# Kernel tuning notes

Measured on AMD Instinct MI355X. Metric: run time of the kernel, lower is better.

## Reference

```python
import jax, jax.numpy as jnp
import numpy as np

K = 3  # Chebyshev order (number of coefficients)


def setup_inputs() -> dict:
    key = jax.random.key(0)
    k1, k2, k3, k4 = jax.random.split(key, 4)
    B, nNode, c_in, T = 16, 512, 32, 64
    c_out = 64
    x = jax.random.normal(k1, (B, nNode, c_in, T), dtype=jnp.float32)
    # scaled Laplacian-like batched adjacency; scale keeps the Chebyshev
    # recursion numerically tame (spectral norm ~ O(1))
    adj = jax.random.normal(k2, (B, nNode, nNode), dtype=jnp.float32) * (1.0 / np.sqrt(nNode))
    # 1x1 conv params: weight [c_out, K*c_in], bias [c_out]
    W = jax.random.normal(k3, (c_out, K * c_in), dtype=jnp.float32) * 0.1
    b = jax.random.normal(k4, (c_out,), dtype=jnp.float32) * 0.1
    return {"x": x, "adj": adj, "W": W, "b": b}


def reference(x, adj, W, b):
    # x: [B, nNode, c_in, T] -> permute(0,2,1,3) -> [B, c_in, nNode, T]
    x = jnp.transpose(x, (0, 2, 1, 3))
    B, c_in, nNode, T = x.shape
    # Chebyshev recursion: L0 = I, L1 = adj, L_k = 2*adj@L_{k-1} - L_{k-2}
    L0 = jnp.broadcast_to(jnp.eye(nNode, dtype=x.dtype), (B, nNode, nNode))
    L1 = adj
    Ls = [L0, L1]
    for _ in range(2, K):
        L2 = 2.0 * jnp.matmul(adj, L1) - L0
        L0, L1 = L1, L2
        Ls.append(L2)
    Lap = jnp.stack(Ls, axis=1)              # [B, K, nNode, nNode]
    Lap = jnp.swapaxes(Lap, -1, -2)          # transpose(-1, -2)
    # einsum 'bcnl,bknq->bckql' then view [B, c_in*K, nNode, T]
    y = jnp.einsum('bcnl,bknq->bckql', x, Lap)  # [B, c_in, K, nNode, T]
    y = y.reshape(B, c_in * K, nNode, T)
    # 1x1 Conv2d: channel mixing + bias
    out = jnp.einsum('oc,bcnl->bonl', W, y) + b[None, :, None, None]
    return out
```

## Files before the change

### kernel.cpp

```cpp
#include <hip/hip_runtime.h>

typedef unsigned short u16;
typedef __bf16 v8bf __attribute__((ext_vector_type(8)));
typedef float f32x4 __attribute__((ext_vector_type(4)));
typedef u16 us8 __attribute__((ext_vector_type(8)));

static __device__ __forceinline__ u16 f2bf(float f) {
  union { __bf16 h; u16 u; } cv;
  cv.h = (__bf16)f;
  return cv.u;
}

__global__ __launch_bounds__(256)
void cvt_f2bf_k(const float* __restrict__ in, u16* __restrict__ out, int n8) {
  const int i = blockIdx.x * 256 + threadIdx.x;
  if (i >= n8) return;
  const float4 a = ((const float4*)in)[2 * i];
  const float4 b = ((const float4*)in)[2 * i + 1];
  us8 r;
  r[0] = f2bf(a.x); r[1] = f2bf(a.y); r[2] = f2bf(a.z); r[3] = f2bf(a.w);
  r[4] = f2bf(b.x); r[5] = f2bf(b.y); r[6] = f2bf(b.z); r[7] = f2bf(b.w);
  ((us8*)out)[i] = r;
}

__global__ __launch_bounds__(256)
void foldw_k(const float* __restrict__ W, u16* __restrict__ Mb) {
  const int i = blockIdx.x * 256 + threadIdx.x;
  if (i >= 64 * 96) return;
  const int cc = i % 96;
  const int r = cc % 3;
  const float w = W[i];
  const float m = (r == 0) ? (w - W[i + 2]) : ((r == 1) ? w : 2.0f * w);
  Mb[i] = f2bf(m);
}

#define BM 128
#define BN 128
#define BK 32

__global__ __launch_bounds__(256)
void gemm_bf16(const u16* __restrict__ A, const u16* __restrict__ Bm,
               u16* __restrict__ C) {
  const int b = blockIdx.z;
  const int row0 = blockIdx.y * BM;
  const int col0 = blockIdx.x * BN;
  const u16* Ab = A + (size_t)b * 512 * 512;
  const u16* Bb = Bm + (size_t)b * 512 * 2048;
  u16* Cb = C + (size_t)b * 512 * 2048;

  __shared__ u16 As[BM][BK + 8];
  __shared__ u16 Bs[BN][BK + 8];

  const int tid = threadIdx.x;
  const int lane = tid & 63;
  const int w = tid >> 6;
  const int wm = (w >> 1) * 64;
  const int wn = (w & 1) * 64;
  const int l16 = lane & 15;
  const int kg = lane >> 4;

  f32x4 acc[4][4];
#pragma unroll
  for (int m = 0; m < 4; ++m)
#pragma unroll
    for (int n = 0; n < 4; ++n)
      acc[m][n] = (f32x4){0.f, 0.f, 0.f, 0.f};

  for (int k0 = 0; k0 < 512; k0 += BK) {
#pragma unroll
    for (int i = 0; i < 2; ++i) {
      const int idx = tid + 256 * i;
      const int r = idx >> 2;
      const int ka = (idx & 3) * 8;
      *(uint4*)&As[r][ka] = *(const uint4*)(Ab + (size_t)(row0 + r) * 512 + k0 + ka);
    }
#pragma unroll
    for (int i = 0; i < 2; ++i) {
      const int idx = tid + 256 * i;
      const int n = idx & 127;
      const int kb = (idx >> 7) * 8;
      const u16* src = Bb + (size_t)(k0 + kb) * 2048 + col0 + n;
      us8 v;
#pragma unroll
      for (int j = 0; j < 8; ++j) v[j] = src[(size_t)j * 2048];
      *(us8*)&Bs[n][kb] = v;
    }
    __syncthreads();
    v8bf af[4], bfr[4];
#pragma unroll
    for (int m = 0; m < 4; ++m) af[m] = *(const v8bf*)&As[wm + m * 16 + l16][kg * 8];
#pragma unroll
    for (int n = 0; n < 4; ++n) bfr[n] = *(const v8bf*)&Bs[wn + n * 16 + l16][kg * 8];
#pragma unroll
    for (int m = 0; m < 4; ++m)
#pragma unroll
      for (int n = 0; n < 4; ++n)
        acc[m][n] = __builtin_amdgcn_mfma_f32_16x16x32_bf16(af[m], bfr[n], acc[m][n], 0, 0, 0);
    __syncthreads();
  }
#pragma unroll
  for (int m = 0; m < 4; ++m)
#pragma unroll
    for (int n = 0; n < 4; ++n)
#pragma unroll
      for (int v = 0; v < 4; ++v) {
        const int rr = row0 + wm + m * 16 + kg * 4 + v;
        const int cc = col0 + wn + n * 16 + l16;
        Cb[(size_t)rr * 2048 + cc] = f2bf(acc[m][n][v]);
      }
}

__global__ __launch_bounds__(256)
void mix_mfma(const float* __restrict__ x0, const u16* __restrict__ x1,
              const u16* __restrict__ y2, const u16* __restrict__ Mb,
              const float* __restrict__ bias, float* __restrict__ out) {
  const int q = blockIdx.x;
  const int b = blockIdx.y;
  __shared__ u16 Vt[64][104];
  __shared__ u16 Ms[64][104];
  const int tid = threadIdx.x;
  const int lane = tid & 63;
  const int w = tid >> 6;
  const int l16 = lane & 15;
  const int kg = lane >> 4;

#pragma unroll
  for (int i = 0; i < 3; ++i) {
    const int idx = tid + 256 * i;
    const int o = idx / 12;
    const int c8 = (idx % 12) * 8;
    *(uint4*)&Ms[o][c8] = *(const uint4*)(Mb + o * 96 + c8);
  }
  const size_t base = ((size_t)b * 512 + q) * 2048;
#pragma unroll
  for (int i = 0; i < 2; ++i) {
    const int idx = tid + 256 * i;
    const int c = idx >> 4;
    const int l0 = (idx & 15) * 4;
    const float4 v = *(const float4*)(x0 + base + c * 64 + l0);
    Vt[l0 + 0][3 * c] = f2bf(v.x);
    Vt[l0 + 1][3 * c] = f2bf(v.y);
    Vt[l0 + 2][3 * c] = f2bf(v.z);
    Vt[l0 + 3][3 * c] = f2bf(v.w);
  }
  {
    const int c = tid >> 3;
    const int l0 = (tid & 7) * 8;
    const us8 v1 = *(const us8*)(x1 + base + c * 64 + l0);
    const us8 v2 = *(const us8*)(y2 + base + c * 64 + l0);
#pragma unroll
    for (int j = 0; j < 8; ++j) {
      Vt[l0 + j][3 * c + 1] = v1[j];
      Vt[l0 + j][3 * c + 2] = v2[j];
    }
  }
  __syncthreads();

  f32x4 acc[4];
#pragma unroll
  for (int n = 0; n < 4; ++n) acc[n] = (f32x4){0.f, 0.f, 0.f, 0.f};
#pragma unroll
  for (int ks = 0; ks < 3; ++ks) {
    const v8bf a = *(const v8bf*)&Ms[w * 16 + l16][ks * 32 + kg * 8];
#pragma unroll
    for (int n = 0; n < 4; ++n) {
      const v8bf bv = *(const v8bf*)&Vt[n * 16 + l16][ks * 32 + kg * 8];
      acc[n] = __builtin_amdgcn_mfma_f32_16x16x32_bf16(a, bv, acc[n], 0, 0, 0);
    }
  }
#pragma unroll
  for (int n = 0; n < 4; ++n)
#pragma unroll
    for (int v = 0; v < 4; ++v) {
      const int o = w * 16 + kg * 4 + v;
      out[(((size_t)b * 64 + o) * 512 + q) * 64 + n * 16 + l16] = acc[n][v] + bias[o];
    }
}

extern "C" void kernel_launch(void* const* d_in, const int* in_sizes, int n_in,
                              void* d_out, int out_size, void* d_ws, size_t ws_size,
                              hipStream_t stream) {
  const float* x   = (const float*)d_in[0];
  const float* adj = (const float*)d_in[1];
  const float* W   = (const float*)d_in[2];
  const float* bia = (const float*)d_in[3];
  float* out = (float*)d_out;

  u16* adj_bf = (u16*)d_ws;
  u16* x_bf   = adj_bf + (size_t)16 * 512 * 512;
  u16* X1     = x_bf   + (size_t)16 * 512 * 2048;
  u16* Y2     = X1     + (size_t)16 * 512 * 2048;
  u16* Mb     = Y2     + (size_t)16 * 512 * 2048;

  const int n8_adj = 16 * 512 * 512 / 8;
  const int n8_x   = 16 * 512 * 2048 / 8;
  hipLaunchKernelGGL(cvt_f2bf_k, dim3(n8_adj / 256), dim3(256), 0, stream, adj, adj_bf, n8_adj);
  hipLaunchKernelGGL(cvt_f2bf_k, dim3(n8_x / 256), dim3(256), 0, stream, x, x_bf, n8_x);
  hipLaunchKernelGGL(foldw_k, dim3(24), dim3(256), 0, stream, W, Mb);

  dim3 gg(2048 / BN, 512 / BM, 16);
  hipLaunchKernelGGL(gemm_bf16, gg, dim3(256), 0, stream, adj_bf, x_bf, X1);
  hipLaunchKernelGGL(gemm_bf16, gg, dim3(256), 0, stream, adj_bf, X1, Y2);

  hipLaunchKernelGGL(mix_mfma, dim3(512, 16), dim3(256), 0, stream, x, X1, Y2, Mb, bia, out);
}
```

Baseline: 151.2 us.

## Store GEMM B operands transposed and load tiles via global_load_lds

x is converted to bf16 in a transposed [B,2048,512] layout, and the first GEMM also writes a transposed copy of X1. Both GEMMs can then fetch K-contiguous tiles with direct global-to-LDS 16-byte loads (BK=64) instead of strided 2-byte gathers across 2048-wide rows. The adj conversion and weight folding are merged into one launch. The cost is an extra transpose pass through LDS, an extra X1T write, and unpadded LDS tiles that may cause bank conflicts.

Result: slower. 158.5 us (+4.8%).

```diff
diff --git a/kernel.cpp b/kernel.cpp
--- a/kernel.cpp
+++ b/kernel.cpp
@@ -4,6 +4,7 @@
 typedef __bf16 v8bf __attribute__((ext_vector_type(8)));
 typedef float f32x4 __attribute__((ext_vector_type(4)));
 typedef u16 us8 __attribute__((ext_vector_type(8)));
+typedef u16 us4 __attribute__((ext_vector_type(4)));
 
 static __device__ __forceinline__ u16 f2bf(float f) {
   union { __bf16 h; u16 u; } cv;
@@ -11,45 +12,77 @@
   return cv.u;
 }
 
-__global__ __launch_bounds__(256)
-void cvt_f2bf_k(const float* __restrict__ in, u16* __restrict__ out, int n8) {
-  const int i = blockIdx.x * 256 + threadIdx.x;
-  if (i >= n8) return;
-  const float4 a = ((const float4*)in)[2 * i];
-  const float4 b = ((const float4*)in)[2 * i + 1];
-  us8 r;
-  r[0] = f2bf(a.x); r[1] = f2bf(a.y); r[2] = f2bf(a.z); r[3] = f2bf(a.w);
-  r[4] = f2bf(b.x); r[5] = f2bf(b.y); r[6] = f2bf(b.z); r[7] = f2bf(b.w);
-  ((us8*)out)[i] = r;
-}
-
-__global__ __launch_bounds__(256)
-void foldw_k(const float* __restrict__ W, u16* __restrict__ Mb) {
-  const int i = blockIdx.x * 256 + threadIdx.x;
-  if (i >= 64 * 96) return;
-  const int cc = i % 96;
-  const int r = cc % 3;
-  const float w = W[i];
-  const float m = (r == 0) ? (w - W[i + 2]) : ((r == 1) ? w : 2.0f * w);
-  Mb[i] = f2bf(m);
-}
-
-#define BM 128
-#define BN 128
-#define BK 32
-
-__global__ __launch_bounds__(256)
-void gemm_bf16(const u16* __restrict__ A, const u16* __restrict__ Bm,
-               u16* __restrict__ C) {
+static __device__ __forceinline__ void gl_lds16(const u16* g, u16* l) {
+  __builtin_amdgcn_global_load_lds(
+      (const __attribute__((address_space(1))) unsigned int*)g,
+      (__attribute__((address_space(3))) unsigned int*)l, 16, 0, 0);
+}
+
+__global__ __launch_bounds__(256)
+void cvt_adj_foldw_k(const float* __restrict__ adj, u16* __restrict__ adj_bf,
+                     const float* __restrict__ W, u16* __restrict__ Mb) {
+  if (blockIdx.x < 2048) {
+    const int i = blockIdx.x * 256 + threadIdx.x;
+    const float4 a = ((const float4*)adj)[2 * i];
+    const float4 b = ((const float4*)adj)[2 * i + 1];
+    us8 r;
+    r[0] = f2bf(a.x); r[1] = f2bf(a.y); r[2] = f2bf(a.z); r[3] = f2bf(a.w);
+    r[4] = f2bf(b.x); r[5] = f2bf(b.y); r[6] = f2bf(b.z); r[7] = f2bf(b.w);
+    ((us8*)adj_bf)[i] = r;
+  } else {
+    for (int i = threadIdx.x; i < 64 * 96; i += 256) {
+      const int cc = i % 96;
+      const int r = cc % 3;
+      const float w = W[i];
+      const float m = (r == 0) ? (w - W[i + 2]) : ((r == 1) ? w : 2.0f * w);
+      Mb[i] = f2bf(m);
+    }
+  }
+}
+
+__global__ __launch_bounds__(256)
+void cvtT_x_k(const float* __restrict__ x, u16* __restrict__ xT) {
+  const int j0 = blockIdx.x * 64;
+  const int q0 = blockIdx.y * 64;
   const int b = blockIdx.z;
-  const int row0 = blockIdx.y * BM;
-  const int col0 = blockIdx.x * BN;
+  __shared__ u16 Ls[64][68];
+  const int tid = threadIdx.x;
+#pragma unroll
+  for (int i = 0; i < 4; ++i) {
+    const int idx = tid + 256 * i;
+    const int r = idx >> 4;
+    const int j4 = (idx & 15) * 4;
+    const float4 v = *(const float4*)(x + ((size_t)(b * 512 + q0 + r) * 2048 + j0 + j4));
+    us4 o;
+    o[0] = f2bf(v.x); o[1] = f2bf(v.y); o[2] = f2bf(v.z); o[3] = f2bf(v.w);
+    *(us4*)&Ls[r][j4] = o;
+  }
+  __syncthreads();
+#pragma unroll
+  for (int i = 0; i < 2; ++i) {
+    const int idx = tid + 256 * i;
+    const int rp = idx >> 3;
+    const int q8 = (idx & 7) * 8;
+    us8 o;
+#pragma unroll
+    for (int j = 0; j < 8; ++j) o[j] = Ls[q8 + j][rp];
+    *(us8*)(xT + ((size_t)(b * 2048 + j0 + rp) * 512 + q0 + q8)) = o;
+  }
+}
+
+template<bool WT>
+__global__ __launch_bounds__(256)
+void gemm_t(const u16* __restrict__ A, const u16* __restrict__ BT,
+            u16* __restrict__ C, u16* __restrict__ CT) {
+  const int b = blockIdx.z;
+  const int row0 = blockIdx.y * 128;
+  const int col0 = blockIdx.x * 128;
   const u16* Ab = A + (size_t)b * 512 * 512;
-  const u16* Bb = Bm + (size_t)b * 512 * 2048;
-  u16* Cb = C + (size_t)b * 512 * 2048;
-
-  __shared__ u16 As[BM][BK + 8];
-  __shared__ u16 Bs[BN][BK + 8];
+  const u16* BTb = BT + (size_t)b * 2048 * 512;
+
+  __shared__ u16 smem[17408];
+  u16* As = smem;
+  u16* Bs = smem + 8192;
 
   const int tid = threadIdx.x;
   const int lane = tid & 63;
@@ -63,41 +96,38 @@
 #pragma unroll
   for (int m = 0; m < 4; ++m)
 #pragma unroll
-    for (int n = 0; n < 4; ++n)
-      acc[m][n] = (f32x4){0.f, 0.f, 0.f, 0.f};
-
-  for (int k0 = 0; k0 < 512; k0 += BK) {
-#pragma unroll
-    for (int i = 0; i < 2; ++i) {
-      const int idx = tid + 256 * i;
-      const int r = idx >> 2;
-      const int ka = (idx & 3) * 8;
-      *(uint4*)&As[r][ka] = *(const uint4*)(Ab + (size_t)(row0 + r) * 512 + k0 + ka);
-    }
-#pragma unroll
-    for (int i = 0; i < 2; ++i) {
-      const int idx = tid + 256 * i;
-      const int n = idx & 127;
-      const int kb = (idx >> 7) * 8;
-      const u16* src = Bb + (size_t)(k0 + kb) * 2048 + col0 + n;
-      us8 v;
-#pragma unroll
-      for (int j = 0; j < 8; ++j) v[j] = src[(size_t)j * 2048];
-      *(us8*)&Bs[n][kb] = v;
-    }
-    __syncthreads();
-    v8bf af[4], bfr[4];
-#pragma unroll
-    for (int m = 0; m < 4; ++m) af[m] = *(const v8bf*)&As[wm + m * 16 + l16][kg * 8];
-#pragma unroll
-    for (int n = 0; n < 4; ++n) bfr[n] = *(const v8bf*)&Bs[wn + n * 16 + l16][kg * 8];
-#pragma unroll
-    for (int m = 0; m < 4; ++m)
+    for (int n = 0; n < 4; ++n) acc[m][n] = (f32x4){0.f, 0.f, 0.f, 0.f};
+
+  for (int k0 = 0; k0 < 512; k0 += 64) {
+    __syncthreads();
+#pragma unroll
+    for (int i = 0; i < 4; ++i) {
+      const int eb = w * 2048 + i * 512;
+      const int e = eb + lane * 8;
+      const int r = e >> 6;
+      const int kk = e & 63;
+      gl_lds16(Ab + (size_t)(row0 + r) * 512 + k0 + kk, As + eb);
+      gl_lds16(BTb + (size_t)(col0 + r) * 512 + k0 + kk, Bs + eb);
+    }
+    __syncthreads();
+#pragma unroll
+    for (int ks = 0; ks < 2; ++ks) {
+      v8bf af[4], bfr[4];
+#pragma unroll
+      for (int m = 0; m < 4; ++m)
+        af[m] = *(const v8bf*)(As + (wm + m * 16 + l16) * 64 + ks * 32 + kg * 8);
 #pragma unroll
       for (int n = 0; n < 4; ++n)
-        acc[m][n] = __builtin_amdgcn_mfma_f32_16x16x32_bf16(af[m], bfr[n], acc[m][n], 0, 0, 0);
-    __syncthreads();
-  }
+        bfr[n] = *(const v8bf*)(Bs + (wn + n * 16 + l16) * 64 + ks * 32 + kg * 8);
+#pragma unroll
+      for (int m = 0; m < 4; ++m)
+#pragma unroll
+        for (int n = 0; n < 4; ++n)
+          acc[m][n] = __builtin_amdgcn_mfma_f32_16x16x32_bf16(af[m], bfr[n], acc[m][n], 0, 0, 0);
+    }
+  }
+
+  u16* Cb = C + (size_t)b * 512 * 2048;
 #pragma unroll
   for (int m = 0; m < 4; ++m)
 #pragma unroll
@@ -108,6 +138,28 @@
         const int cc = col0 + wn + n * 16 + l16;
         Cb[(size_t)rr * 2048 + cc] = f2bf(acc[m][n][v]);
       }
+
+  if constexpr (WT) {
+    __syncthreads();
+    u16* Ctr = smem;
+#pragma unroll
+    for (int m = 0; m < 4; ++m)
+#pragma unroll
+      for (int n = 0; n < 4; ++n)
+#pragma unroll
+        for (int v = 0; v < 4; ++v)
+          Ctr[(wn + n * 16 + l16) * 136 + (wm + m * 16 + kg * 4 + v)] = f2bf(acc[m][n][v]);
+    __syncthreads();
+    u16* CTb = CT + (size_t)b * 2048 * 512;
+#pragma unroll
+    for (int i = 0; i < 8; ++i) {
+      const int idx = tid + 256 * i;
+      const int jp = idx >> 4;
+      const int q8 = (idx & 15) * 8;
+      const us8 o = *(const us8*)(Ctr + jp * 136 + q8);
+      *(us8*)(CTb + (size_t)(col0 + jp) * 512 + row0 + q8) = o;
+    }
+  }
 }
 
 __global__ __launch_bounds__(256)
@@ -187,20 +239,18 @@
   float* out = (float*)d_out;
 
   u16* adj_bf = (u16*)d_ws;
-  u16* x_bf   = adj_bf + (size_t)16 * 512 * 512;
-  u16* X1     = x_bf   + (size_t)16 * 512 * 2048;
-  u16* Y2     = X1     + (size_t)16 * 512 * 2048;
+  u16* xT     = adj_bf + (size_t)16 * 512 * 512;
+  u16* X1     = xT     + (size_t)16 * 2048 * 512;
+  u16* X1T    = X1     + (size_t)16 * 512 * 2048;
+  u16* Y2     = X1T    + (size_t)16 * 2048 * 512;
   u16* Mb     = Y2     + (size_t)16 * 512 * 2048;
 
-  const int n8_adj = 16 * 512 * 512 / 8;
-  const int n8_x   = 16 * 512 * 2048 / 8;
-  hipLaunchKernelGGL(cvt_f2bf_k, dim3(n8_adj / 256), dim3(256), 0, stream, adj, adj_bf, n8_adj);
-  hipLaunchKernelGGL(cvt_f2bf_k, dim3(n8_x / 256), dim3(256), 0, stream, x, x_bf, n8_x);
-  hipLaunchKernelGGL(foldw_k, dim3(24), dim3(256), 0, stream, W, Mb);
-
-  dim3 gg(2048 / BN, 512 / BM, 16);
-  hipLaunchKernelGGL(gemm_bf16, gg, dim3(256), 0, stream, adj_bf, x_bf, X1);
-  hipLaunchKernelGGL(gemm_bf16, gg, dim3(256), 0, stream, adj_bf, X1, Y2);
+  hipLaunchKernelGGL(cvt_adj_foldw_k, dim3(2049), dim3(256), 0, stream, adj, adj_bf, W, Mb);
+  hipLaunchKernelGGL(cvtT_x_k, dim3(32, 8, 16), dim3(256), 0, stream, x, xT);
+
+  dim3 gg(2048 / 128, 512 / 128, 16);
+  hipLaunchKernelGGL((gemm_t<true>), gg, dim3(256), 0, stream, adj_bf, xT, X1, X1T);
+  hipLaunchKernelGGL((gemm_t<false>), gg, dim3(256), 0, stream, adj_bf, X1T, Y2, (u16*)nullptr);
 
   hipLaunchKernelGGL(mix_mfma, dim3(512, 16), dim3(256), 0, stream, x, X1, Y2, Mb, bia, out);
 }
```
